# Performance work log

Measured on AMD Instinct MI355X. Metric: run time of the kernel, lower is better.

The kernel has to match this reference:

```python
import jax, jax.numpy as jnp
import numpy as np

B, N, D_IN, D_OUT = 8, 2048, 64, 64
ALPHA = 0.2          # LeakyReLU negative slope
MASK_FILL = -9e15    # matches -9000000000000000.0 in the torch code
P_EDGE = 0.05


def _build_adj(key):
    # base random adjacency [N,N], then block structure [[adj, I],[0, adj]]
    base = (jax.random.uniform(key, (N, N)) < P_EDGE).astype(jnp.float32)
    eye = jnp.eye(N, dtype=jnp.float32)
    top = jnp.concatenate([base, eye], axis=1)
    bot = jnp.concatenate([jnp.zeros((N, N), jnp.float32), base], axis=1)
    return jnp.concatenate([top, bot], axis=0)  # [2N, 2N]


def setup_inputs() -> dict:
    key = jax.random.key(0)
    k1, k2, k3, k4, k5, k6 = jax.random.split(key, 6)
    h = jax.random.normal(k1, (B, N, D_IN), jnp.float32)
    ht = jax.random.normal(k2, (B, N, D_IN), jnp.float32)
    # xavier_uniform-ish scale for params
    W = jax.random.normal(k3, (D_IN, D_OUT), jnp.float32) * 0.15
    a1 = jax.random.normal(k4, (D_OUT, 1), jnp.float32) * 0.15
    a2 = jax.random.normal(k5, (D_OUT, 1), jnp.float32) * 0.15
    adj = _build_adj(k6)
    return {"h": h, "ht": ht, "W": W, "a1": a1, "a2": a2, "adj": adj}


def reference(h, ht, W, a1, a2, adj):
    # concat along node dim: [b, 2n, d_in]
    hc = jnp.concatenate([ht, h], axis=1)
    Wh = jnp.einsum('bni,io->bno', hc, W)           # [b, 2n, d_out]
    # additive attention scores: Wh1_i + Wh2_j, LeakyReLU
    Wh1 = Wh @ a1                                    # [b, 2n, 1]
    Wh2 = Wh @ a2                                    # [b, 2n, 1]
    e = Wh1 + jnp.swapaxes(Wh2, 1, 2)                # [b, 2n, 2n]
    e = jnp.where(e > 0, e, ALPHA * e)               # LeakyReLU
    att = jnp.where(adj > 0, e, MASK_FILL)
    att = jax.nn.softmax(att, axis=1)                # NOTE: dim=1 as in torch code
    # dropout is identity in eval mode
    hp = jnp.matmul(att, Wh)                         # [b, 2n, d_out]
    n = adj.shape[0] // 2
    hp = jnp.concatenate([hp[:, :n], hp[:, n:]], axis=-1)  # [b, n, 2*d_out]
    return jax.nn.elu(hp)                            # concat=True -> ELU
```

## Files before the change

kernel.cpp:

```cpp
#include <hip/hip_runtime.h>
#include <hip/hip_bf16.h>
#include <math.h>

#define BB 8
#define NN 2048
#define TN 4096
#define DD 64

typedef __attribute__((ext_vector_type(8))) short short8;
typedef __attribute__((ext_vector_type(4))) float f32x4;
typedef __attribute__((ext_vector_type(4))) unsigned int u32x4;

__device__ __forceinline__ unsigned short f2bf(float f) {
    union { float f; unsigned int i; } v; v.f = f;
    unsigned int r = v.i + 0x7FFF + ((v.i >> 16) & 1);
    return (unsigned short)(r >> 16);
}
__device__ __forceinline__ float bf2f(unsigned short u) {
    union { unsigned int i; float f; } v; v.i = ((unsigned int)u) << 16; return v.f;
}

__global__ __launch_bounds__(256, 4) void k1_wh(
                      const float* __restrict__ h,
                      const float* __restrict__ ht,
                      const float* __restrict__ W,
                      const float* __restrict__ a1,
                      const float* __restrict__ a2,
                      float* __restrict__ Wh,
                      float* __restrict__ E1p, float* __restrict__ E1n,
                      float* __restrict__ E2p, float* __restrict__ E2n,
                      float* __restrict__ E1i) {
    __shared__ float xs[4][512];
    int tid = threadIdx.x;
    int w = tid >> 6, l = tid & 63;
    float wreg[64];
    #pragma unroll
    for (int k = 0; k < 64; ++k) wreg[k] = W[k * 64 + l];
    float a1l = a1[l], a2l = a2[l];
    int rowbase = (blockIdx.x * 4 + w) * 8;
    int b = rowbase >> 12;
    int m0 = rowbase & (TN - 1);
    const float* srcw = (m0 < NN) ? (ht + ((size_t)b * NN + m0) * DD)
                                  : (h  + ((size_t)b * NN + (m0 - NN)) * DD);
    f32x4 g0 = *reinterpret_cast<const f32x4*>(srcw + l * 8);
    f32x4 g1 = *reinterpret_cast<const f32x4*>(srcw + l * 8 + 4);
    *reinterpret_cast<f32x4*>(&xs[w][l * 8])     = g0;
    *reinterpret_cast<f32x4*>(&xs[w][l * 8 + 4]) = g1;
    __syncthreads();
    for (int r = 0; r < 8; ++r) {
        const f32x4* xr = reinterpret_cast<const f32x4*>(&xs[w][r * 64]);
        float c0 = 0.f, c1 = 0.f, c2 = 0.f, c3 = 0.f;
        #pragma unroll
        for (int k = 0; k < 16; ++k) {
            f32x4 s = xr[k];
            c0 += s[0] * wreg[k * 4 + 0];
            c1 += s[1] * wreg[k * 4 + 1];
            c2 += s[2] * wreg[k * 4 + 2];
            c3 += s[3] * wreg[k * 4 + 3];
        }
        float acc = (c0 + c1) + (c2 + c3);
        int m = m0 + r;
        Wh[((size_t)b * TN + m) * DD + l] = acc;
        float r1 = acc * a1l;
        float r2 = acc * a2l;
        #pragma unroll
        for (int off = 32; off > 0; off >>= 1) {
            r1 += __shfl_xor(r1, off, 64);
            r2 += __shfl_xor(r2, off, 64);
        }
        if (l == 0) {
            size_t o = (size_t)b * TN + m;
            float pp = __expf(r1), pn = __expf(0.2f * r1);
            E1p[o] = pp;
            E1n[o] = pn;
            int sp = (b < 4) ? b       : 8 + (b - 4);
            int sn = (b < 4) ? 4 + b   : 12 + (b - 4);
            E1i[(size_t)m * 16 + sp] = pp;
            E1i[(size_t)m * 16 + sn] = pn;
            E2p[o] = __expf(r2);
            E2n[o] = __expf(0.2f * r2);
        }
    }
}

__global__ __launch_bounds__(256) void k2_mask_stats(
    const float* __restrict__ adj,
    const float* __restrict__ E1i,
    const float* __restrict__ E2p, const float* __restrict__ E2n,
    unsigned long long* __restrict__ qmask,
    float* __restrict__ Spart) {
    int tid = threadIdx.x;
    int w = tid >> 6, l = tid & 63;
    int half = blockIdx.z;
    int j = half * 2048 + blockIdx.x * 256 + tid;
    int i0 = half * 2048 + blockIdx.y * 32;
    f32x4 e2p0, e2p1, e2n0, e2n1;
    #pragma unroll
    for (int b = 0; b < 4; ++b) {
        e2p0[b] = E2p[(size_t)b * TN + j];
        e2n0[b] = E2n[(size_t)b * TN + j];
        e2p1[b] = E2p[(size_t)(b + 4) * TN + j];
        e2n1[b] = E2n[(size_t)(b + 4) * TN + j];
    }
    f32x4 acc0 = {0.f, 0.f, 0.f, 0.f}, acc1 = {0.f, 0.f, 0.f, 0.f};
    const f32x4* e1 = reinterpret_cast<const f32x4*>(E1i + (size_t)i0 * 16);
    for (int it8 = 0; it8 < 4; ++it8) {
        float avv[8];
        #pragma unroll
        for (int k = 0; k < 8; ++k)
            avv[k] = adj[(size_t)(i0 + it8 * 8 + k) * TN + j];
        #pragma unroll
        for (int k = 0; k < 8; ++k) {
            int ii = it8 * 8 + k;
            unsigned long long bal = __ballot(avv[k] != 0.f);
            if (l == 0)
                qmask[(size_t)(i0 + ii) * 32 + blockIdx.x * 4 + w] = bal;
            f32x4 P0 = e1[ii * 4 + 0];
            f32x4 N0 = e1[ii * 4 + 1];
            f32x4 P1 = e1[ii * 4 + 2];
            f32x4 N1 = e1[ii * 4 + 3];
            f32x4 v0 = __builtin_elementwise_max(P0 * e2p0, N0 * e2n0);
            f32x4 v1 = __builtin_elementwise_max(P1 * e2p1, N1 * e2n1);
            acc0 += v0 * avv[k];
            acc1 += v1 * avv[k];
        }
    }
    #pragma unroll
    for (int b = 0; b < 4; ++b) {
        Spart[((size_t)blockIdx.y * 8 + b) * TN + j]     = acc0[b];
        Spart[((size_t)blockIdx.y * 8 + b + 4) * TN + j] = acc1[b];
    }
}

__global__ __launch_bounds__(256) void k3_whn(
    const float* __restrict__ Wh,
    const float* __restrict__ Spart,
    const float* __restrict__ E1p, const float* __restrict__ E1n,
    const float* __restrict__ E2p, const float* __restrict__ E2n,
    unsigned short* __restrict__ Wt) {
    __shared__ float tile[64][65];
    __shared__ float ps[4][64];
    __shared__ float rs[64];
    int b = blockIdx.y;
    int j0 = blockIdx.x * 64;
    int tid = threadIdx.x;
    int jj = tid & 63, part = tid >> 6;
    float s = 0.f;
    #pragma unroll
    for (int k = 0; k < 16; ++k) {
        int strip = part * 16 + k;
        s += Spart[((size_t)strip * 8 + b) * TN + j0 + jj];
    }
    ps[part][jj] = s;
    __syncthreads();
    if (tid < 64) {
        float tot = ps[0][tid] + ps[1][tid] + ps[2][tid] + ps[3][tid];
        int j = j0 + tid;
        if (j >= NN) {
            int i = j - NN;
            tot += fmaxf(E1p[(size_t)b * TN + i] * E2p[(size_t)b * TN + j],
                         E1n[(size_t)b * TN + i] * E2n[(size_t)b * TN + j]);
        }
        rs[tid] = 1.0f / tot;
    }
    for (int e = tid; e < 4096; e += 256) {
        int jt = e >> 6, d = e & 63;
        tile[jt][d] = Wh[((size_t)b * TN + j0 + jt) * DD + d];
    }
    __syncthreads();
    for (int e = tid; e < 512; e += 256) {
        int d = e >> 3, jg = e & 7;
        union { unsigned short u[8]; short8 s8; } pk;
        #pragma unroll
        for (int k = 0; k < 8; ++k) {
            int jt = jg * 8 + k;
            pk.u[k] = f2bf(tile[jt][d] * rs[jt]);
        }
        *reinterpret_cast<short8*>(Wt + ((size_t)b * DD + d) * TN + j0 + jg * 8) = pk.s8;
    }
}

__global__ __launch_bounds__(256) void k4_pv(
    const unsigned int* __restrict__ qmask32,
    const float* __restrict__ E1p, const float* __restrict__ E1n,
    const float* __restrict__ E2p, const float* __restrict__ E2n,
    const unsigned short* __restrict__ Wt,
    unsigned short* __restrict__ hpq) {
    __shared__ unsigned short wt_s[64 * 140];
    int bx = blockIdx.x;
    int b  = bx & 7;
    int js = (bx >> 3) & 3;
    int it = bx >> 5;
    int i0 = it * 64;
    int half = (it >= 32);
    int tid = threadIdx.x;
    int w = tid >> 6, l = tid & 63;
    int m = l & 15, q = l >> 4;
    int irow = i0 + w * 16 + m;
    float e1p_v = E1p[(size_t)b * TN + irow];
    float e1n_v = E1n[(size_t)b * TN + irow];
    const float* e2pb = E2p + (size_t)b * TN;
    const float* e2nb = E2n + (size_t)b * TN;
    const unsigned short* wtb = Wt + (size_t)b * DD * TN;
    const unsigned int* mrow = qmask32 + (size_t)irow * 64;

    int r0 = tid >> 4, c0 = tid & 15;
    const int jbase = half * 2048 + js * 512;
    const int jloc0 = js * 512;

    f32x4 acc[4];
    #pragma unroll
    for (int dt = 0; dt < 4; ++dt) acc[dt] = (f32x4){0.f, 0.f, 0.f, 0.f};

    short8 g[4];
    #pragma unroll
    for (int k = 0; k < 4; ++k)
        g[k] = *reinterpret_cast<const short8*>(
            wtb + (size_t)(r0 + 16 * k) * TN + jbase + c0 * 8);

    for (int jt = 0; jt < 4; ++jt) {
        int j0 = jbase + jt * 128;
        __syncthreads();
        #pragma unroll
        for (int k = 0; k < 4; ++k)
            *reinterpret_cast<short8*>(&wt_s[(r0 + 16 * k) * 140 + c0 * 8]) = g[k];
        if (jt < 3) {
            #pragma unroll
            for (int k = 0; k < 4; ++k)
                g[k] = *reinterpret_cast<const short8*>(
                    wtb + (size_t)(r0 + 16 * k) * TN + j0 + 128 + c0 * 8);
        }
        u32x4 m4 = *reinterpret_cast<const u32x4*>(mrow + ((jloc0 + jt * 128) >> 5));
        __syncthreads();

        #pragma unroll
        for (int t = 0; t < 4; ++t) {
            int jb = j0 + t * 32 + q * 8;
            unsigned int bytev = (m4[t] >> (q * 8)) & 0xFFu;
            f32x4 p20 = *reinterpret_cast<const f32x4*>(e2pb + jb);
            f32x4 p21 = *reinterpret_cast<const f32x4*>(e2pb + jb + 4);
            f32x4 n20 = *reinterpret_cast<const f32x4*>(e2nb + jb);
            f32x4 n21 = *reinterpret_cast<const f32x4*>(e2nb + jb + 4);
            f32x4 v0 = __builtin_elementwise_max(p20 * e1p_v, n20 * e1n_v);
            f32x4 v1 = __builtin_elementwise_max(p21 * e1p_v, n21 * e1n_v);
            union { f32x4 f; u32x4 u; } uv0, uv1;
            uv0.f = v0; uv1.f = v1;
            u32x4 mk0, mk1;
            #pragma unroll
            for (int c = 0; c < 4; ++c) {
                mk0[c] = (unsigned int)((int)(bytev << (31 - c)) >> 31);
                mk1[c] = (unsigned int)((int)(bytev << (27 - c)) >> 31);
            }
            uv0.u &= mk0; uv1.u &= mk1;
            union { unsigned int u[4]; short8 s8; } af;
            __hip_bfloat162 hb0 = __float22bfloat162_rn(make_float2(uv0.f[0], uv0.f[1]));
            __hip_bfloat162 hb1 = __float22bfloat162_rn(make_float2(uv0.f[2], uv0.f[3]));
            __hip_bfloat162 hb2 = __float22bfloat162_rn(make_float2(uv1.f[0], uv1.f[1]));
            __hip_bfloat162 hb3 = __float22bfloat162_rn(make_float2(uv1.f[2], uv1.f[3]));
            af.u[0] = *reinterpret_cast<unsigned int*>(&hb0);
            af.u[1] = *reinterpret_cast<unsigned int*>(&hb1);
            af.u[2] = *reinterpret_cast<unsigned int*>(&hb2);
            af.u[3] = *reinterpret_cast<unsigned int*>(&hb3);
            #pragma unroll
            for (int dt = 0; dt < 4; ++dt) {
                short8 bf = *reinterpret_cast<const short8*>(
                    &wt_s[(dt * 16 + m) * 140 + t * 32 + q * 8]);
                acc[dt] = __builtin_amdgcn_mfma_f32_16x16x32_bf16(af.s8, bf, acc[dt], 0, 0, 0);
            }
        }
    }

    int gbase = i0 + w * 16 + q * 4;
    if (half == 0 && js == 0) {
        #pragma unroll
        for (int r = 0; r < 4; ++r) {
            int gg = gbase + r;
            float ed = fmaxf(E1p[(size_t)b * TN + gg] * e2pb[gg + NN],
                             E1n[(size_t)b * TN + gg] * e2nb[gg + NN]);
            #pragma unroll
            for (int dt = 0; dt < 4; ++dt) {
                int d = dt * 16 + m;
                acc[dt][r] += ed * bf2f(wtb[(size_t)d * TN + gg + NN]);
            }
        }
    }

    union { unsigned int u[8]; u32x4 v[2]; } pk;
    #pragma unroll
    for (int dt = 0; dt < 4; ++dt) {
        __hip_bfloat162 p0 = __float22bfloat162_rn(make_float2(acc[dt][0], acc[dt][1]));
        __hip_bfloat162 p1 = __float22bfloat162_rn(make_float2(acc[dt][2], acc[dt][3]));
        pk.u[dt * 2 + 0] = *reinterpret_cast<unsigned int*>(&p0);
        pk.u[dt * 2 + 1] = *reinterpret_cast<unsigned int*>(&p1);
    }
    unsigned short* hp = hpq +
        (((((size_t)js * 8 + b) * 64 + it) * 4 + w) * 64 + l) * 16;
    *reinterpret_cast<u32x4*>(hp)     = pk.v[0];
    *reinterpret_cast<u32x4*>(hp + 8) = pk.v[1];
}

__global__ void k5_epi(const unsigned short* __restrict__ hpq,
                       float* __restrict__ out) {
    int t = blockIdx.x * 256 + threadIdx.x;
    int d4 = t & 31;
    int n = (t >> 5) & 2047;
    int b = t >> 16;
    int g, sd;
    if (d4 < 16) { g = n;        sd = d4 * 4; }
    else         { g = n + NN;   sd = (d4 - 16) * 4; }
    int it = g >> 6, w = (g >> 4) & 3, q = (g >> 2) & 3, r = g & 3;
    int dt = sd >> 4, m0 = sd & 15;
    const size_t JSTR = (size_t)8 * 64 * 4 * 64 * 16;
    size_t base = ((((size_t)b * 64 + it) * 4 + w) * 64 + q * 16) * 16 + dt * 4 + r;
    f32x4 s = {0.f, 0.f, 0.f, 0.f};
    #pragma unroll
    for (int js = 0; js < 4; ++js) {
        const unsigned short* p = hpq + js * JSTR + base;
        #pragma unroll
        for (int c = 0; c < 4; ++c) s[c] += bf2f(p[(size_t)(m0 + c) * 16]);
    }
    f32x4 rr;
    #pragma unroll
    for (int c = 0; c < 4; ++c) rr[c] = (s[c] > 0.f) ? s[c] : expm1f(s[c]);
    *reinterpret_cast<f32x4*>(out + ((size_t)b * NN + n) * 128 + d4 * 4) = rr;
}

extern "C" void kernel_launch(void* const* d_in, const int* in_sizes, int n_in,
                              void* d_out, int out_size, void* d_ws, size_t ws_size,
                              hipStream_t stream) {
    const float* h   = (const float*)d_in[0];
    const float* ht  = (const float*)d_in[1];
    const float* W   = (const float*)d_in[2];
    const float* a1  = (const float*)d_in[3];
    const float* a2  = (const float*)d_in[4];
    const float* adj = (const float*)d_in[5];
    float* out = (float*)d_out;

    char* ws = (char*)d_ws;
    float* Wh          = (float*)(ws);
    float* Spart       = (float*)(ws + (8 << 20));
    unsigned short* Wt = (unsigned short*)(ws + (16 << 20));
    float* E1p         = (float*)(ws + (20 << 20));
    float* E1n         = (float*)(ws + (20 << 20) + (128 << 10));
    float* E2p         = (float*)(ws + (20 << 20) + (256 << 10));
    float* E2n         = (float*)(ws + (20 << 20) + (384 << 10));
    unsigned long long* qmask = (unsigned long long*)(ws + (20 << 20) + (512 << 10));
    float* E1i         = (float*)(ws + (20 << 20) + (512 << 10) + (2 << 20));
    const unsigned int* qmask32 = (const unsigned int*)qmask;
    unsigned short* hpq = (unsigned short*)ws;

    k1_wh<<<dim3(BB * TN / 32), dim3(256), 0, stream>>>(h, ht, W, a1, a2, Wh,
                                                        E1p, E1n, E2p, E2n, E1i);
    k2_mask_stats<<<dim3(8, 64, 2), dim3(256), 0, stream>>>(adj, E1i, E2p, E2n,
                                                            qmask, Spart);
    k3_whn<<<dim3(64, 8), dim3(256), 0, stream>>>(Wh, Spart, E1p, E1n, E2p, E2n, Wt);
    k4_pv<<<dim3(2048), dim3(256), 0, stream>>>(qmask32, E1p, E1n, E2p, E2n, Wt,
                                                hpq);
    k5_epi<<<dim3(2048), dim3(256), 0, stream>>>(hpq, out);
}
```

Measured before the change: 170.6 us.

## Fuse split-K reduction and ELU epilogue into PV kernel, drop separate epilogue kernel

```diff
diff --git a/kernel.cpp b/kernel.cpp
--- a/kernel.cpp
+++ b/kernel.cpp
@@ -180,23 +180,25 @@
     }
 }
 
-__global__ __launch_bounds__(256) void k4_pv(
+__global__ __launch_bounds__(512) void k4_pv(
     const unsigned int* __restrict__ qmask32,
     const float* __restrict__ E1p, const float* __restrict__ E1n,
     const float* __restrict__ E2p, const float* __restrict__ E2n,
     const unsigned short* __restrict__ Wt,
-    unsigned short* __restrict__ hpq) {
-    __shared__ unsigned short wt_s[64 * 140];
+    float* __restrict__ out) {
+    __shared__ unsigned short wt_s[2][64 * 140];
+    __shared__ float red[4 * 64 * 16];
     int bx = blockIdx.x;
     int b  = bx & 7;
-    int js = (bx >> 3) & 3;
-    int it = bx >> 5;
+    int it = bx >> 3;
     int i0 = it * 64;
     int half = (it >= 32);
     int tid = threadIdx.x;
     int w = tid >> 6, l = tid & 63;
+    int wg = w >> 2;
+    int wr = w & 3;
     int m = l & 15, q = l >> 4;
-    int irow = i0 + w * 16 + m;
+    int irow = i0 + wr * 16 + m;
     float e1p_v = E1p[(size_t)b * TN + irow];
     float e1n_v = E1n[(size_t)b * TN + irow];
     const float* e2pb = E2p + (size_t)b * TN;
@@ -204,9 +206,11 @@
     const unsigned short* wtb = Wt + (size_t)b * DD * TN;
     const unsigned int* mrow = qmask32 + (size_t)irow * 64;
 
-    int r0 = tid >> 4, c0 = tid & 15;
-    const int jbase = half * 2048 + js * 512;
-    const int jloc0 = js * 512;
+    int tt = tid & 255;
+    int r0 = tt >> 4, c0 = tt & 15;
+    const int jbase = half * 2048 + wg * 1024;
+    const int jloc0 = wg * 1024;
+    unsigned short* ws_ = &wt_s[wg][0];
 
     f32x4 acc[4];
     #pragma unroll
@@ -218,13 +222,13 @@
         g[k] = *reinterpret_cast<const short8*>(
             wtb + (size_t)(r0 + 16 * k) * TN + jbase + c0 * 8);
 
-    for (int jt = 0; jt < 4; ++jt) {
+    for (int jt = 0; jt < 8; ++jt) {
         int j0 = jbase + jt * 128;
         __syncthreads();
         #pragma unroll
         for (int k = 0; k < 4; ++k)
-            *reinterpret_cast<short8*>(&wt_s[(r0 + 16 * k) * 140 + c0 * 8]) = g[k];
-        if (jt < 3) {
+            *reinterpret_cast<short8*>(&ws_[(r0 + 16 * k) * 140 + c0 * 8]) = g[k];
+        if (jt < 7) {
             #pragma unroll
             for (int k = 0; k < 4; ++k)
                 g[k] = *reinterpret_cast<const short8*>(
@@ -264,65 +268,56 @@
             #pragma unroll
             for (int dt = 0; dt < 4; ++dt) {
                 short8 bf = *reinterpret_cast<const short8*>(
-                    &wt_s[(dt * 16 + m) * 140 + t * 32 + q * 8]);
+                    &ws_[(dt * 16 + m) * 140 + t * 32 + q * 8]);
                 acc[dt] = __builtin_amdgcn_mfma_f32_16x16x32_bf16(af.s8, bf, acc[dt], 0, 0, 0);
             }
         }
     }
 
-    int gbase = i0 + w * 16 + q * 4;
-    if (half == 0 && js == 0) {
+    __syncthreads();
+    if (wg == 1) {
+        #pragma unroll
+        for (int dt = 0; dt < 4; ++dt) {
+            #pragma unroll
+            for (int r = 0; r < 4; ++r)
+                red[((wr * 64 + l) * 16) + dt * 4 + r] = acc[dt][r];
+        }
+    }
+    __syncthreads();
+    if (wg == 0) {
+        #pragma unroll
+        for (int dt = 0; dt < 4; ++dt) {
+            #pragma unroll
+            for (int r = 0; r < 4; ++r)
+                acc[dt][r] += red[((wr * 64 + l) * 16) + dt * 4 + r];
+        }
+        int gbase = i0 + wr * 16 + q * 4;
+        if (half == 0) {
+            #pragma unroll
+            for (int r = 0; r < 4; ++r) {
+                int gg = gbase + r;
+                float ed = fmaxf(E1p[(size_t)b * TN + gg] * e2pb[gg + NN],
+                                 E1n[(size_t)b * TN + gg] * e2nb[gg + NN]);
+                #pragma unroll
+                for (int dt = 0; dt < 4; ++dt) {
+                    int d = dt * 16 + m;
+                    acc[dt][r] += ed * bf2f(wtb[(size_t)d * TN + gg + NN]);
+                }
+            }
+        }
+        int ch_base = half ? 64 : 0;
         #pragma unroll
         for (int r = 0; r < 4; ++r) {
             int gg = gbase + r;
-            float ed = fmaxf(E1p[(size_t)b * TN + gg] * e2pb[gg + NN],
-                             E1n[(size_t)b * TN + gg] * e2nb[gg + NN]);
+            int n = gg - half * NN;
+            float* orow = out + ((size_t)b * NN + n) * 128 + ch_base;
             #pragma unroll
             for (int dt = 0; dt < 4; ++dt) {
-                int d = dt * 16 + m;
-                acc[dt][r] += ed * bf2f(wtb[(size_t)d * TN + gg + NN]);
+                float v = acc[dt][r];
+                orow[dt * 16 + m] = (v > 0.f) ? v : expm1f(v);
             }
         }
     }
-
-    union { unsigned int u[8]; u32x4 v[2]; } pk;
-    #pragma unroll
-    for (int dt = 0; dt < 4; ++dt) {
-        __hip_bfloat162 p0 = __float22bfloat162_rn(make_float2(acc[dt][0], acc[dt][1]));
-        __hip_bfloat162 p1 = __float22bfloat162_rn(make_float2(acc[dt][2], acc[dt][3]));
-        pk.u[dt * 2 + 0] = *reinterpret_cast<unsigned int*>(&p0);
-        pk.u[dt * 2 + 1] = *reinterpret_cast<unsigned int*>(&p1);
-    }
-    unsigned short* hp = hpq +
-        (((((size_t)js * 8 + b) * 64 + it) * 4 + w) * 64 + l) * 16;
-    *reinterpret_cast<u32x4*>(hp)     = pk.v[0];
-    *reinterpret_cast<u32x4*>(hp + 8) = pk.v[1];
-}
-
-__global__ void k5_epi(const unsigned short* __restrict__ hpq,
-                       float* __restrict__ out) {
-    int t = blockIdx.x * 256 + threadIdx.x;
-    int d4 = t & 31;
-    int n = (t >> 5) & 2047;
-    int b = t >> 16;
-    int g, sd;
-    if (d4 < 16) { g = n;        sd = d4 * 4; }
-    else         { g = n + NN;   sd = (d4 - 16) * 4; }
-    int it = g >> 6, w = (g >> 4) & 3, q = (g >> 2) & 3, r = g & 3;
-    int dt = sd >> 4, m0 = sd & 15;
-    const size_t JSTR = (size_t)8 * 64 * 4 * 64 * 16;
-    size_t base = ((((size_t)b * 64 + it) * 4 + w) * 64 + q * 16) * 16 + dt * 4 + r;
-    f32x4 s = {0.f, 0.f, 0.f, 0.f};
-    #pragma unroll
-    for (int js = 0; js < 4; ++js) {
-        const unsigned short* p = hpq + js * JSTR + base;
-        #pragma unroll
-        for (int c = 0; c < 4; ++c) s[c] += bf2f(p[(size_t)(m0 + c) * 16]);
-    }
-    f32x4 rr;
-    #pragma unroll
-    for (int c = 0; c < 4; ++c) rr[c] = (s[c] > 0.f) ? s[c] : expm1f(s[c]);
-    *reinterpret_cast<f32x4*>(out + ((size_t)b * NN + n) * 128 + d4 * 4) = rr;
 }
 
 extern "C" void kernel_launch(void* const* d_in, const int* in_sizes, int n_in,
@@ -347,14 +342,12 @@
     unsigned long long* qmask = (unsigned long long*)(ws + (20 << 20) + (512 << 10));
     float* E1i         = (float*)(ws + (20 << 20) + (512 << 10) + (2 << 20));
     const unsigned int* qmask32 = (const unsigned int*)qmask;
-    unsigned short* hpq = (unsigned short*)ws;
 
     k1_wh<<<dim3(BB * TN / 32), dim3(256), 0, stream>>>(h, ht, W, a1, a2, Wh,
                                                         E1p, E1n, E2p, E2n, E1i);
     k2_mask_stats<<<dim3(8, 64, 2), dim3(256), 0, stream>>>(adj, E1i, E2p, E2n,
                                                             qmask, Spart);
     k3_whn<<<dim3(64, 8), dim3(256), 0, stream>>>(Wh, Spart, E1p, E1n, E2p, E2n, Wt);
-    k4_pv<<<dim3(2048), dim3(256), 0, stream>>>(qmask32, E1p, E1n, E2p, E2n, Wt,
-                                                hpq);
-    k5_epi<<<dim3(2048), dim3(256), 0, stream>>>(hpq, out);
-}
+    k4_pv<<<dim3(512), dim3(512), 0, stream>>>(qmask32, E1p, E1n, E2p, E2n, Wt,
+                                               out);
+}
```

Measured after the change: 199.2 us. +16.8%, slower.
